# Kernel optimization log

Measured on AMD Instinct MI355X. Metric: run time of the kernel, lower is better.

## Reference

```python
import jax, jax.numpy as jnp
import numpy as np

B, N, DIM = 16, 784, 512
H, KD, VD = 8, 64, 256  # num_heads, key_dim, val_dim (attn_ratio=4)
RES = 28
EPS = 1e-5
SCALE = KD ** -0.5


def _make_bias_idxs():
    # pos: [2, N] grid coordinates; rel_pos[0]*RES + rel_pos[1]
    yy, xx = np.meshgrid(np.arange(RES), np.arange(RES), indexing='ij')
    pos = np.stack([yy.reshape(-1), xx.reshape(-1)])  # [2, N]
    rel = np.abs(pos[:, :, None] - pos[:, None, :])   # [2, N, N]
    return jnp.asarray(rel[0] * RES + rel[1], dtype=jnp.int32)


def _bn(x, gamma, beta, mean, var):
    return (x - mean) * (gamma * jax.lax.rsqrt(var + EPS)) + beta


def setup_inputs() -> dict:
    key = jax.random.key(0)
    ks = jax.random.split(key, 12)
    qkv_out = (2 * KD + VD) * H  # 3072
    return {
        'x': jax.random.normal(ks[0], (B, N, DIM), jnp.float32),
        'qkv_w': jax.random.normal(ks[1], (qkv_out, DIM), jnp.float32) * (DIM ** -0.5),
        'qkv_gamma': jax.random.uniform(ks[2], (qkv_out,), jnp.float32, 0.5, 1.5),
        'qkv_beta': jax.random.normal(ks[3], (qkv_out,), jnp.float32) * 0.1,
        'qkv_mean': jax.random.normal(ks[4], (qkv_out,), jnp.float32) * 0.1,
        'qkv_var': jax.random.uniform(ks[5], (qkv_out,), jnp.float32, 0.5, 1.5),
        'attention_biases': jax.random.normal(ks[6], (H, RES * RES), jnp.float32) * 0.02,
        'proj_w': jax.random.normal(ks[7], (DIM, VD * H), jnp.float32) * ((VD * H) ** -0.5),
        'proj_gamma': jax.random.uniform(ks[8], (DIM,), jnp.float32, 0.5, 1.5),
        'proj_beta': jax.random.normal(ks[9], (DIM,), jnp.float32) * 0.1,
        'proj_mean': jax.random.normal(ks[10], (DIM,), jnp.float32) * 0.1,
        'proj_var': jax.random.uniform(ks[11], (DIM,), jnp.float32, 0.5, 1.5),
        'bias_idxs': _make_bias_idxs(),
    }


def reference(x, qkv_w, qkv_gamma, qkv_beta, qkv_mean, qkv_var,
              attention_biases, proj_w, proj_gamma, proj_beta,
              proj_mean, proj_var, bias_idxs):
    # QKV: Linear (no bias) + BatchNorm1d (eval/fused form)
    qkv = _bn(jnp.einsum('bnc,oc->bno', x, qkv_w),
              qkv_gamma, qkv_beta, qkv_mean, qkv_var)        # [B, N, 3072]
    qkv = qkv.reshape(B, N, H, 2 * KD + VD)
    q = qkv[..., :KD].transpose(0, 2, 1, 3)                  # [B, H, N, KD]
    k = qkv[..., KD:2 * KD].transpose(0, 2, 1, 3)            # [B, H, N, KD]
    v = qkv[..., 2 * KD:].transpose(0, 2, 1, 3)              # [B, H, N, VD]

    bias = attention_biases[:, bias_idxs]                    # [H, N, N]
    attn = jnp.einsum('bhnd,bhmd->bhnm', q, k) * SCALE + bias
    attn = jax.nn.softmax(attn, axis=-1)
    out = jnp.einsum('bhnm,bhmd->bhnd', attn, v)             # [B, H, N, VD]
    out = out.transpose(0, 2, 1, 3).reshape(B, N, H * VD)    # [B, N, 2048]

    # proj: SiLU -> Linear (no bias) -> BN (eval/fused form)
    out = jax.nn.silu(out)
    out = _bn(jnp.einsum('bnv,cv->bnc', out, proj_w),
              proj_gamma, proj_beta, proj_mean, proj_var)    # [B, N, DIM]
    return out
```

## Files before the change

### kernel.cpp

```cpp
#include <hip/hip_runtime.h>

#define Bsz 16
#define Nseq 784
#define DIM 512
#define NH 8
#define KD 64
#define VD 256
#define QKV_OUT 3072
#define HV 2048
#define NN 614656

typedef __attribute__((ext_vector_type(8))) short short8;
typedef __attribute__((ext_vector_type(4))) short short4v;
typedef __attribute__((ext_vector_type(4))) float floatx4;
typedef __attribute__((ext_vector_type(16))) float f32x16;
typedef __attribute__((ext_vector_type(2))) unsigned u32x2;

#define OSTR 136

#if __has_builtin(__builtin_amdgcn_exp2f)
#define EXP2(x) __builtin_amdgcn_exp2f(x)
#else
#define EXP2(x) exp2f(x)
#endif

__device__ __forceinline__ unsigned short f2bf(float f) {
  union { float f; unsigned u; } v; v.f = f;
  unsigned r = v.u + 0x7fffu + ((v.u >> 16) & 1u);
  return (unsigned short)(r >> 16);
}
__device__ __forceinline__ float bfLO(unsigned u) {
  union { unsigned u; float f; } v; v.u = u << 16; return v.f;
}
__device__ __forceinline__ float bfHI(unsigned u) {
  union { unsigned u; float f; } v; v.u = u & 0xffff0000u; return v.f;
}

__device__ __forceinline__ void glds16(const unsigned short* g, unsigned short* l) {
  __builtin_amdgcn_global_load_lds(
      (const __attribute__((address_space(1))) void*)g,
      (__attribute__((address_space(3))) void*)l, 16, 0, 0);
}

#define N4X 1605632
#define N4Q 393216
#define N4P 262144
__global__ void cvt_all_kernel(const float* __restrict__ x,
                               const float* __restrict__ qw,
                               const float* __restrict__ pw,
                               unsigned short* __restrict__ xb,
                               unsigned short* __restrict__ wq,
                               unsigned short* __restrict__ wp) {
  int i = blockIdx.x * 256 + threadIdx.x;
  const float4* s; ushort4* d; int off;
  if (i < N4X)              { s = (const float4*)x;  d = (ushort4*)xb; off = i; }
  else if (i < N4X + N4Q)   { s = (const float4*)qw; d = (ushort4*)wq; off = i - N4X; }
  else if (i < N4X + N4Q + N4P) { s = (const float4*)pw; d = (ushort4*)wp; off = i - N4X - N4Q; }
  else return;
  float4 v = s[off];
  ushort4 o;
  o.x = f2bf(v.x); o.y = f2bf(v.y); o.z = f2bf(v.z); o.w = f2bf(v.w);
  d[off] = o;
}

__global__ void bias_pre_kernel(const float* __restrict__ biases,
                                const int* __restrict__ bias_idxs,
                                unsigned short* __restrict__ bias_tab) {
  int t = blockIdx.x * 256 + threadIdx.x;
  if (t >= NN) return;
  int idx = bias_idxs[t];
  for (int h = 0; h < NH; ++h)
    bias_tab[(size_t)h * NN + t] = f2bf(1.44269504f * biases[h * Nseq + idx]);
}

__global__ __launch_bounds__(256, 2) void qkv_gemm_kernel(
    const unsigned short* __restrict__ A,
    const unsigned short* __restrict__ Bw,
    const float* __restrict__ gamma, const float* __restrict__ beta,
    const float* __restrict__ mean,  const float* __restrict__ var,
    unsigned short* __restrict__ qo,
    unsigned short* __restrict__ ko,
    unsigned short* __restrict__ vto)
{
  const int K = DIM;
  __shared__ unsigned short smem[128 * OSTR];
  int tid = threadIdx.x;
  int wave = tid >> 6, lane = tid & 63;
  int quad = lane >> 4, l16 = lane & 15;
  int wm = wave >> 1, wn = wave & 1;
  int m0 = blockIdx.y * 128, n0 = blockIdx.x * 128;

  int srow = wave * 32 + (lane >> 2);
  int sch = (lane & 3) * 8;
  const unsigned short* Ab = A + (size_t)(m0 + srow) * K + sch;
  const unsigned short* Bb = Bw + (size_t)(n0 + srow) * K + sch;
  unsigned short* AsW = &smem[wave * 1024];
  unsigned short* BsW = &smem[4096 + wave * 1024];

  floatx4 acc[4][4];
  for (int i = 0; i < 4; ++i)
    for (int j = 0; j < 4; ++j) acc[i][j] = (floatx4)0.0f;

  glds16(Ab, AsW);
  glds16(Ab + 16 * K, AsW + 512);
  glds16(Bb, BsW);
  glds16(Bb + 16 * K, BsW + 512);

  for (int k = 0; k < 16; ++k) {
    int cur = k & 1, nb = cur ^ 1;
    __builtin_amdgcn_s_waitcnt(0xC07F);
    __builtin_amdgcn_s_barrier();
    int k0n = ((k + 1) & 15) * 32;
    glds16(Ab + k0n, AsW + nb * 8192);
    glds16(Ab + k0n + 16 * K, AsW + nb * 8192 + 512);
    glds16(Bb + k0n, BsW + nb * 8192);
    glds16(Bb + k0n + 16 * K, BsW + nb * 8192 + 512);
    __builtin_amdgcn_s_waitcnt(0x0F74);
    __builtin_amdgcn_s_barrier();

    const unsigned short* As = &smem[cur * 8192];
    const unsigned short* Bs = &smem[4096 + cur * 8192];
    short8 af[4], bfr[4];
    for (int mt = 0; mt < 4; ++mt)
      af[mt] = *(const short8*)&As[(wm * 64 + mt * 16 + l16) * 32 + quad * 8];
    for (int nt = 0; nt < 4; ++nt)
      bfr[nt] = *(const short8*)&Bs[(wn * 64 + nt * 16 + l16) * 32 + quad * 8];
    for (int mt = 0; mt < 4; ++mt)
      for (int nt = 0; nt < 4; ++nt)
        acc[mt][nt] = __builtin_amdgcn_mfma_f32_16x16x32_bf16(af[mt], bfr[nt], acc[mt][nt], 0, 0, 0);
  }

  int tt = n0 % 384;
  int h = n0 / 384;
  __builtin_amdgcn_s_waitcnt(0x0070);
  __syncthreads();

  if (tt == 0) {
    for (int nt = 0; nt < 4; ++nt) {
      int o = n0 + wn * 64 + nt * 16 + l16;
      float sc = gamma[o] * rsqrtf(var[o] + 1e-5f);
      float bb = beta[o] - mean[o] * sc;
      if (wn == 0) { sc *= 0.18033688f; bb *= 0.18033688f; }
      int jl = wn * 64 + nt * 16 + l16;
      for (int mt = 0; mt < 4; ++mt)
        for (int r = 0; r < 4; ++r) {
          int ml = wm * 64 + mt * 16 + quad * 4 + r;
          smem[ml * OSTR + jl] = f2bf(acc[mt][nt][r] * sc + bb);
        }
    }
    __syncthreads();
    for (int i = 0; i < 8; ++i) {
      int c = i * 256 + tid;
      int ml = c >> 4, jc = c & 15;
      int m = m0 + ml;
      int b = m / 784, n = m - b * 784;
      uint4 v = *(uint4*)&smem[ml * OSTR + jc * 8];
      int j = jc * 8;
      if (j < 64) *(uint4*)&qo[(((size_t)b * NH + h) * Nseq + n) * KD + j] = v;
      else        *(uint4*)&ko[(((size_t)b * NH + h) * Nseq + n) * KD + (j - 64)] = v;
    }
  } else {
    for (int nt = 0; nt < 4; ++nt) {
      int o = n0 + wn * 64 + nt * 16 + l16;
      float sc = gamma[o] * rsqrtf(var[o] + 1e-5f);
      float bb = beta[o] - mean[o] * sc;
      int cl = wn * 64 + nt * 16 + l16;
      for (int mt = 0; mt < 4; ++mt)
        for (int r = 0; r < 4; ++r) {
          int ml = wm * 64 + mt * 16 + quad * 4 + r;
          smem[cl * OSTR + ml] = f2bf(acc[mt][nt][r] * sc + bb);
        }
    }
    __syncthreads();
    int cbase = tt - 128;
    for (int i = 0; i < 8; ++i) {
      int c = i * 256 + tid;
      int cl = c >> 4, mc = c & 15;
      int m = m0 + mc * 8;
      int b = m / 784, n = m - b * 784;
      uint4 v = *(uint4*)&smem[cl * OSTR + mc * 8];
      *(uint4*)&vto[(((size_t)b * NH + h) * VD + cbase + cl) * Nseq + n] = v;
    }
  }
}

__global__ __launch_bounds__(256, 2) void attn_kernel(
    const unsigned short* __restrict__ qb,
    const unsigned short* __restrict__ kb,
    const unsigned short* __restrict__ vtb,
    const unsigned short* __restrict__ bias_tab,
    unsigned short* __restrict__ U)
{
  __shared__ unsigned short vt_lds[2 * 256 * 64];
  __shared__ unsigned short k_lds[2 * 64 * 64];
  int tid = threadIdx.x;
  int wave = tid >> 6, lane = tid & 63;
  int lo = lane & 31, hi = lane >> 5;

  int L = blockIdx.x;
  int xcd = L & 7;
  int s = L >> 3;
  int qp = s % 7;
  int bg = s / 7;
  int bh = bg * 8 + xcd;
  int b = bg, h = xcd;

  int qrow_g = qp * 128 + wave * 32 + lo;
  int qrow = qrow_g < Nseq ? qrow_g : Nseq - 1;

  int lc = lane >> 3;
  int lch = (lane & 7) ^ lc;
  int swz = lo & 7;

  const unsigned short* vsrc = vtb + ((size_t)bh * VD + wave * 64 + lc) * Nseq + lch * 8;
  const unsigned short* ksrc = kb + ((size_t)bh * Nseq + wave * 16 + lc) * KD + lch * 8;
  const unsigned short* brow = bias_tab + (size_t)h * NN + (size_t)qrow * Nseq + hi * 4;

  short8 qf[4];
  {
    const unsigned short* qp_ = qb + ((size_t)bh * Nseq + qrow) * KD + hi * 8;
#pragma unroll
    for (int kst = 0; kst < 4; ++kst) qf[kst] = *(const short8*)(qp_ + kst * 16);
  }

#pragma unroll
  for (int i = 0; i < 8; ++i) glds16(vsrc + i * (8 * Nseq), &vt_lds[wave * 4096 + i * 512]);
  glds16(ksrc, &k_lds[wave * 1024]);
  glds16(ksrc + 8 * KD, &k_lds[wave * 1024 + 512]);
  u32x2 bvC[8], bvN[8];
#pragma unroll
  for (int t = 0; t < 8; ++t) bvC[t] = *(const u32x2*)(brow + t * 8);

  f32x16 oacc[8];
#pragma unroll
  for (int ct = 0; ct < 8; ++ct) oacc[ct] = (f32x16)0.0f;
  float lsum = 0.0f;

  for (int kt = 0; kt < 13; ++kt) {
    int cur = kt & 1, nb = cur ^ 1;
    __builtin_amdgcn_s_waitcnt(0xC07F);
    __builtin_amdgcn_s_barrier();
    int ktn = kt + 1; if (ktn >= 13) ktn = 0;
#pragma unroll
    for (int i = 0; i < 8; ++i)
      glds16(vsrc + i * (8 * Nseq) + ktn * 64, &vt_lds[nb * 16384 + wave * 4096 + i * 512]);
    glds16(ksrc + ktn * (64 * KD), &k_lds[nb * 4096 + wave * 1024]);
    glds16(ksrc + ktn * (64 * KD) + 8 * KD, &k_lds[nb * 4096 + wave * 1024 + 512]);
#pragma unroll
    for (int t = 0; t < 8; ++t) bvN[t] = *(const u32x2*)(brow + ktn * 64 + t * 8);
    __builtin_amdgcn_s_waitcnt(0x4F72);
    __builtin_amdgcn_s_barrier();
    __builtin_amdgcn_sched_barrier(0);

    const unsigned short* kbuf = &k_lds[cur * 4096];
    const unsigned short* vbuf = &vt_lds[cur * 16384];

    f32x16 st0, st1;
#pragma unroll
    for (int r = 0; r < 16; ++r) {
      unsigned c0 = bvC[r >> 2][(r & 3) >> 1];
      unsigned c1 = bvC[4 + (r >> 2)][(r & 3) >> 1];
      st0[r] = (r & 1) ? bfHI(c0) : bfLO(c0);
      st1[r] = (r & 1) ? bfHI(c1) : bfLO(c1);
    }
#pragma unroll
    for (int kst = 0; kst < 4; ++kst) {
      int ch = ((kst * 2 + hi) ^ swz) * 8;
      short8 kf0 = *(const short8*)&kbuf[lo * 64 + ch];
      short8 kf1 = *(const short8*)&kbuf[(32 + lo) * 64 + ch];
      st0 = __builtin_amdgcn_mfma_f32_32x32x16_bf16(kf0, qf[kst], st0, 0, 0, 0);
      st1 = __builtin_amdgcn_mfma_f32_32x32x16_bf16(kf1, qf[kst], st1, 0, 0, 0);
    }

#pragma unroll
    for (int r = 0; r < 16; ++r) st0[r] = EXP2(st0[r]);
#pragma unroll
    for (int r = 0; r < 16; ++r) st1[r] = EXP2(st1[r]);
    if (kt == 12) {
#pragma unroll
      for (int r = 8; r < 16; ++r) st0[r] = 0.0f;
#pragma unroll
      for (int r = 0; r < 16; ++r) st1[r] = 0.0f;
    }
    {
      float s0 = (st0[0] + st0[1]) + (st0[2] + st0[3]);
      float s1 = (st0[4] + st0[5]) + (st0[6] + st0[7]);
      float s2 = (st0[8] + st0[9]) + (st0[10] + st0[11]);
      float s3 = (st0[12] + st0[13]) + (st0[14] + st0[15]);
      float s4 = (st1[0] + st1[1]) + (st1[2] + st1[3]);
      float s5 = (st1[4] + st1[5]) + (st1[6] + st1[7]);
      float s6 = (st1[8] + st1[9]) + (st1[10] + st1[11]);
      float s7 = (st1[12] + st1[13]) + (st1[14] + st1[15]);
      lsum += ((s0 + s1) + (s2 + s3)) + ((s4 + s5) + (s6 + s7));
    }

    short8 pf[4];
#pragma unroll
    for (int kst = 0; kst < 4; ++kst) {
      float a0, a1, a2, a3, b0, b1, b2, b3;
      if (kst == 0)      { a0=st0[0]; a1=st0[1]; a2=st0[2];  a3=st0[3];  b0=st0[4];  b1=st0[5];  b2=st0[6];  b3=st0[7];  }
      else if (kst == 1) { a0=st0[8]; a1=st0[9]; a2=st0[10]; a3=st0[11]; b0=st0[12]; b1=st0[13]; b2=st0[14]; b3=st0[15]; }
      else if (kst == 2) { a0=st1[0]; a1=st1[1]; a2=st1[2];  a3=st1[3];  b0=st1[4];  b1=st1[5];  b2=st1[6];  b3=st1[7];  }
      else               { a0=st1[8]; a1=st1[9]; a2=st1[10]; a3=st1[11]; b0=st1[12]; b1=st1[13]; b2=st1[14]; b3=st1[15]; }
      unsigned X0, X1, Y0, Y1;
      asm("v_cvt_pk_bf16_f32 %0, %1, %2" : "=v"(X0) : "v"(a0), "v"(a1));
      asm("v_cvt_pk_bf16_f32 %0, %1, %2" : "=v"(X1) : "v"(a2), "v"(a3));
      asm("v_cvt_pk_bf16_f32 %0, %1, %2" : "=v"(Y0) : "v"(b0), "v"(b1));
      asm("v_cvt_pk_bf16_f32 %0, %1, %2" : "=v"(Y1) : "v"(b2), "v"(b3));
      union { unsigned u[4]; short8 s; } pk_;
      pk_.u[0] = X0; pk_.u[1] = X1; pk_.u[2] = Y0; pk_.u[3] = Y1;
      pf[kst] = pk_.s;
    }

#pragma unroll
    for (int kst = 0; kst < 4; ++kst) {
      int chL = ((kst * 2) ^ swz) * 8 + 4 * hi;
      int chH = ((kst * 2 + 1) ^ swz) * 8 + 4 * hi;
#pragma unroll
      for (int ct = 0; ct < 8; ++ct) {
        const unsigned short* vr = &vbuf[(ct * 32 + lo) * 64];
        union { short4v half[2]; short8 s; } vv;
        vv.half[0] = *(const short4v*)&vr[chL];
        vv.half[1] = *(const short4v*)&vr[chH];
        oacc[ct] = __builtin_amdgcn_mfma_f32_32x32x16_bf16(vv.s, pf[kst], oacc[ct], 0, 0, 0);
      }
    }

#pragma unroll
    for (int t = 0; t < 8; ++t) bvC[t] = bvN[t];
  }

  __builtin_amdgcn_s_waitcnt(0x0070);

  float tot = lsum + __shfl_xor(lsum, 32);
  float inv = 1.0f / tot;
  if (qrow_g < Nseq) {
    size_t base = ((size_t)b * Nseq + qrow_g) * HV + h * VD;
#pragma unroll
    for (int ct = 0; ct < 8; ++ct)
#pragma unroll
      for (int g2 = 0; g2 < 4; ++g2) {
        ushort4 o4;
#pragma unroll
        for (int r4 = 0; r4 < 4; ++r4) {
          float u = oacc[ct][g2 * 4 + r4] * inv;
          float sg = 1.0f / (1.0f + EXP2(-u * 1.44269504f));
          ((unsigned short*)&o4)[r4] = f2bf(u * sg);
        }
        *(ushort4*)&U[base + ct * 32 + g2 * 8 + hi * 4] = o4;
      }
  }
}

__global__ __launch_bounds__(256, 2) void proj_gemm_kernel(
    const unsigned short* __restrict__ Ubuf,
    const unsigned short* __restrict__ Wp,
    const float* __restrict__ gamma, const float* __restrict__ beta,
    const float* __restrict__ mean,  const float* __restrict__ var,
    float* __restrict__ out)
{
  const int K = HV;
  __shared__ unsigned short smem[16384];
  int tid = threadIdx.x;
  int wave = tid >> 6, lane = tid & 63;
  int quad = lane >> 4, l16 = lane & 15;
  int wm = wave >> 1, wn = wave & 1;
  int o0 = blockIdx.y * 128, mB = blockIdx.x * 128;

  int srow = wave * 32 + (lane >> 2);
  int sch = (lane & 3) * 8;
  const unsigned short* Ab = Wp + (size_t)(o0 + srow) * K + sch;
  const unsigned short* Bb = Ubuf + (size_t)(mB + srow) * K + sch;
  unsigned short* AsW = &smem[wave * 1024];
  unsigned short* BsW = &smem[4096 + wave * 1024];

  floatx4 acc[4][4];
  for (int i = 0; i < 4; ++i)
    for (int j = 0; j < 4; ++j) acc[i][j] = (floatx4)0.0f;

  glds16(Ab, AsW);
  glds16(Ab + 16 * K, AsW + 512);
  glds16(Bb, BsW);
  glds16(Bb + 16 * K, BsW + 512);

  for (int k = 0; k < 64; ++k) {
    int cur = k & 1, nb = cur ^ 1;
    __builtin_amdgcn_s_waitcnt(0xC07F);
    __builtin_amdgcn_s_barrier();
    int k0n = ((k + 1) & 63) * 32;
    glds16(Ab + k0n, AsW + nb * 8192);
    glds16(Ab + k0n + 16 * K, AsW + nb * 8192 + 512);
    glds16(Bb + k0n, BsW + nb * 8192);
    glds16(Bb + k0n + 16 * K, BsW + nb * 8192 + 512);
    __builtin_amdgcn_s_waitcnt(0x0F74);
    __builtin_amdgcn_s_barrier();

    const unsigned short* As = &smem[cur * 8192];
    const unsigned short* Bs = &smem[4096 + cur * 8192];
    short8 af[4], bfr[4];
    for (int mt = 0; mt < 4; ++mt)
      af[mt] = *(const short8*)&As[(wm * 64 + mt * 16 + l16) * 32 + quad * 8];
    for (int nt = 0; nt < 4; ++nt)
      bfr[nt] = *(const short8*)&Bs[(wn * 64 + nt * 16 + l16) * 32 + quad * 8];
    for (int mt = 0; mt < 4; ++mt)
      for (int nt = 0; nt < 4; ++nt)
        acc[mt][nt] = __builtin_amdgcn_mfma_f32_16x16x32_bf16(af[mt], bfr[nt], acc[mt][nt], 0, 0, 0);
  }
  __builtin_amdgcn_s_waitcnt(0x0070);

  for (int mt = 0; mt < 4; ++mt) {
    int ob = o0 + wm * 64 + mt * 16 + quad * 4;
    float4 g = *(const float4*)&gamma[ob];
    float4 vr = *(const float4*)&var[ob];
    float4 mn = *(const float4*)&mean[ob];
    float4 bt = *(const float4*)&beta[ob];
    float sc0 = g.x * rsqrtf(vr.x + 1e-5f), bb0 = bt.x - mn.x * sc0;
    float sc1 = g.y * rsqrtf(vr.y + 1e-5f), bb1 = bt.y - mn.y * sc1;
    float sc2 = g.z * rsqrtf(vr.z + 1e-5f), bb2 = bt.z - mn.z * sc2;
    float sc3 = g.w * rsqrtf(vr.w + 1e-5f), bb3 = bt.w - mn.w * sc3;
    for (int nt = 0; nt < 4; ++nt) {
      int m = mB + wn * 64 + nt * 16 + l16;
      float4 v;
      v.x = acc[mt][nt][0] * sc0 + bb0;
      v.y = acc[mt][nt][1] * sc1 + bb1;
      v.z = acc[mt][nt][2] * sc2 + bb2;
      v.w = acc[mt][nt][3] * sc3 + bb3;
      *(float4*)&out[(size_t)m * DIM + ob] = v;
    }
  }
}

extern "C" void kernel_launch(void* const* d_in, const int* in_sizes, int n_in,
                              void* d_out, int out_size, void* d_ws, size_t ws_size,
                              hipStream_t stream) {
  const float* x          = (const float*)d_in[0];
  const float* qkv_w      = (const float*)d_in[1];
  const float* qkv_gamma  = (const float*)d_in[2];
  const float* qkv_beta   = (const float*)d_in[3];
  const float* qkv_mean   = (const float*)d_in[4];
  const float* qkv_var    = (const float*)d_in[5];
  const float* att_biases = (const float*)d_in[6];
  const float* proj_w     = (const float*)d_in[7];
  const float* proj_gamma = (const float*)d_in[8];
  const float* proj_beta  = (const float*)d_in[9];
  const float* proj_mean  = (const float*)d_in[10];
  const float* proj_var   = (const float*)d_in[11];
  const int*   bias_idxs  = (const int*)d_in[12];
  float* out = (float*)d_out;

  char* ws = (char*)d_ws;
  unsigned short* xb  = (unsigned short*)(ws);
  unsigned short* bias_tab = (unsigned short*)(ws);
  unsigned short* wq  = (unsigned short*)(ws + 12845056);
  unsigned short* wp  = (unsigned short*)(ws + 15990784);
  unsigned short* qo  = (unsigned short*)(ws + 18087936);
  unsigned short* ko  = (unsigned short*)(ws + 30932992);
  unsigned short* vto = (unsigned short*)(ws + 43778048);
  unsigned short* Ub  = (unsigned short*)(ws + 95158272);

  {
    int n4 = N4X + N4Q + N4P;
    cvt_all_kernel<<<(n4 + 255) / 256, 256, 0, stream>>>(x, qkv_w, proj_w, xb, wq, wp);
  }

  qkv_gemm_kernel<<<dim3(QKV_OUT / 128, (Bsz * Nseq) / 128), 256, 0, stream>>>(
      xb, wq, qkv_gamma, qkv_beta, qkv_mean, qkv_var, qo, ko, vto);

  bias_pre_kernel<<<(NN + 255) / 256, 256, 0, stream>>>(att_biases, bias_idxs, bias_tab);

  attn_kernel<<<7 * Bsz * NH, 256, 0, stream>>>(qo, ko, vto, bias_tab, Ub);

  proj_gemm_kernel<<<dim3((Bsz * Nseq) / 128, DIM / 128), 256, 0, stream>>>(
      Ub, wp, proj_gamma, proj_beta, proj_mean, proj_var, out);
}
```

Before: 309.3 us.

## Permute V-transpose and bias layouts so attention loads use 16-byte vectors

The V-transpose store in the QKV GEMM and the precomputed bias table are written in a permuted key order. This lets the attention kernel read each V fragment with one 16-byte LDS load instead of two 8-byte loads, and read the bias with four 16-byte global loads instead of eight 8-byte loads. The waitcnt is adjusted to the new load count. s_setprio is also wrapped around the MFMA sections to favour matrix issue. The cost is split 8-byte global stores in the GEMM epilogue, and correctness depends on the permutation matching the MFMA operand order exactly.

```diff
diff --git a/kernel.cpp b/kernel.cpp
--- a/kernel.cpp
+++ b/kernel.cpp
@@ -11,10 +11,9 @@
 #define NN 614656
 
 typedef __attribute__((ext_vector_type(8))) short short8;
-typedef __attribute__((ext_vector_type(4))) short short4v;
 typedef __attribute__((ext_vector_type(4))) float floatx4;
 typedef __attribute__((ext_vector_type(16))) float f32x16;
-typedef __attribute__((ext_vector_type(2))) unsigned u32x2;
+typedef __attribute__((ext_vector_type(4))) unsigned u32x4;
 
 #define OSTR 136
 
@@ -69,8 +68,9 @@
   int t = blockIdx.x * 256 + threadIdx.x;
   if (t >= NN) return;
   int idx = bias_idxs[t];
+  int p = (t & ~12) | ((t & 4) << 1) | ((t & 8) >> 1);
   for (int h = 0; h < NH; ++h)
-    bias_tab[(size_t)h * NN + t] = f2bf(1.44269504f * biases[h * Nseq + idx]);
+    bias_tab[(size_t)h * NN + p] = f2bf(1.44269504f * biases[h * Nseq + idx]);
 }
 
 __global__ __launch_bounds__(256, 2) void qkv_gemm_kernel(
@@ -179,7 +179,10 @@
       int m = m0 + mc * 8;
       int b = m / 784, n = m - b * 784;
       uint4 v = *(uint4*)&smem[cl * OSTR + mc * 8];
-      *(uint4*)&vto[(((size_t)b * NH + h) * VD + cbase + cl) * Nseq + n] = v;
+      size_t rb = (((size_t)b * NH + h) * VD + cbase + cl) * Nseq;
+      int nlo = (n & ~8) | ((n & 8) >> 1);
+      *(uint2*)&vto[rb + nlo]     = make_uint2(v.x, v.y);
+      *(uint2*)&vto[rb + nlo + 8] = make_uint2(v.z, v.w);
     }
   }
 }
@@ -214,7 +217,7 @@
 
   const unsigned short* vsrc = vtb + ((size_t)bh * VD + wave * 64 + lc) * Nseq + lch * 8;
   const unsigned short* ksrc = kb + ((size_t)bh * Nseq + wave * 16 + lc) * KD + lch * 8;
-  const unsigned short* brow = bias_tab + (size_t)h * NN + (size_t)qrow * Nseq + hi * 4;
+  const unsigned short* brow = bias_tab + (size_t)h * NN + (size_t)qrow * Nseq + 8 * hi;
 
   short8 qf[4];
   {
@@ -227,9 +230,9 @@
   for (int i = 0; i < 8; ++i) glds16(vsrc + i * (8 * Nseq), &vt_lds[wave * 4096 + i * 512]);
   glds16(ksrc, &k_lds[wave * 1024]);
   glds16(ksrc + 8 * KD, &k_lds[wave * 1024 + 512]);
-  u32x2 bvC[8], bvN[8];
-#pragma unroll
-  for (int t = 0; t < 8; ++t) bvC[t] = *(const u32x2*)(brow + t * 8);
+  u32x4 bbC[4], bbN[4];
+#pragma unroll
+  for (int g = 0; g < 4; ++g) bbC[g] = *(const u32x4*)(brow + g * 16);
 
   f32x16 oacc[8];
 #pragma unroll
@@ -247,8 +250,8 @@
     glds16(ksrc + ktn * (64 * KD), &k_lds[nb * 4096 + wave * 1024]);
     glds16(ksrc + ktn * (64 * KD) + 8 * KD, &k_lds[nb * 4096 + wave * 1024 + 512]);
 #pragma unroll
-    for (int t = 0; t < 8; ++t) bvN[t] = *(const u32x2*)(brow + ktn * 64 + t * 8);
-    __builtin_amdgcn_s_waitcnt(0x4F72);
+    for (int g = 0; g < 4; ++g) bbN[g] = *(const u32x4*)(brow + ktn * 64 + g * 16);
+    __builtin_amdgcn_s_waitcnt(0x0F7E);
     __builtin_amdgcn_s_barrier();
     __builtin_amdgcn_sched_barrier(0);
 
@@ -258,11 +261,12 @@
     f32x16 st0, st1;
 #pragma unroll
     for (int r = 0; r < 16; ++r) {
-      unsigned c0 = bvC[r >> 2][(r & 3) >> 1];
-      unsigned c1 = bvC[4 + (r >> 2)][(r & 3) >> 1];
+      unsigned c0 = bbC[r >> 3][(r >> 1) & 3];
+      unsigned c1 = bbC[2 + (r >> 3)][(r >> 1) & 3];
       st0[r] = (r & 1) ? bfHI(c0) : bfLO(c0);
       st1[r] = (r & 1) ? bfHI(c1) : bfLO(c1);
     }
+    __builtin_amdgcn_s_setprio(1);
 #pragma unroll
     for (int kst = 0; kst < 4; ++kst) {
       int ch = ((kst * 2 + hi) ^ swz) * 8;
@@ -271,6 +275,7 @@
       st0 = __builtin_amdgcn_mfma_f32_32x32x16_bf16(kf0, qf[kst], st0, 0, 0, 0);
       st1 = __builtin_amdgcn_mfma_f32_32x32x16_bf16(kf1, qf[kst], st1, 0, 0, 0);
     }
+    __builtin_amdgcn_s_setprio(0);
 
 #pragma unroll
     for (int r = 0; r < 16; ++r) st0[r] = EXP2(st0[r]);
@@ -312,22 +317,21 @@
       pf[kst] = pk_.s;
     }
 
+    __builtin_amdgcn_s_setprio(1);
 #pragma unroll
     for (int kst = 0; kst < 4; ++kst) {
-      int chL = ((kst * 2) ^ swz) * 8 + 4 * hi;
-      int chH = ((kst * 2 + 1) ^ swz) * 8 + 4 * hi;
+      int ch = ((kst * 2 + hi) ^ swz) * 8;
+      const unsigned short* vr0 = &vbuf[lo * 64 + ch];
 #pragma unroll
       for (int ct = 0; ct < 8; ++ct) {
-        const unsigned short* vr = &vbuf[(ct * 32 + lo) * 64];
-        union { short4v half[2]; short8 s; } vv;
-        vv.half[0] = *(const short4v*)&vr[chL];
-        vv.half[1] = *(const short4v*)&vr[chH];
-        oacc[ct] = __builtin_amdgcn_mfma_f32_32x32x16_bf16(vv.s, pf[kst], oacc[ct], 0, 0, 0);
+        short8 vf = *(const short8*)&vr0[ct * 2048];
+        oacc[ct] = __builtin_amdgcn_mfma_f32_32x32x16_bf16(vf, pf[kst], oacc[ct], 0, 0, 0);
       }
     }
-
-#pragma unroll
-    for (int t = 0; t < 8; ++t) bvC[t] = bvN[t];
+    __builtin_amdgcn_s_setprio(0);
+
+#pragma unroll
+    for (int g = 0; g < 4; ++g) bbC[g] = bbN[g];
   }
 
   __builtin_amdgcn_s_waitcnt(0x0070);
```

Result: faster. 297.9 us (-3.7%).
